# Kernel tuning notes

Hardware: AMD Instinct MI355X
Metric: run time of the kernel (lower is better)

The kernel has to match this reference:

```python
import jax, jax.numpy as jnp
import numpy as np

B, L, D = 2, 2048, 2048
NUM_HEADS, NUM_KV_HEADS, HEAD_DIM = 8, 4, 256
GROUPS = NUM_HEADS // NUM_KV_HEADS
ROPE_BASE, ROPE_SCALE, ROPE_PROP = 10000.0, 1.0, 1.0
WINDOW = 1024
SOFT_CAP = 50.0
K_MASK = -2.3819763e+38
EPS = 1e-6


def rms_norm(x, scale):
    # RMSNorm(head_dim, with_scale=True, scale_plus_one=False), fp32 internals
    xf = x.astype(jnp.float32)
    var = jnp.mean(jnp.square(xf), axis=-1, keepdims=True)
    return (xf * jax.lax.rsqrt(var + EPS) * scale).astype(x.dtype)


def apply_rope(x, positions):
    # x: [B, L, N, H]; Gemma-style half-split rotation over rope_proportion of H
    H = x.shape[-1]
    rope_dim = int(H * ROPE_PROP)
    half = rope_dim // 2
    freq = ROPE_BASE ** (2.0 * jnp.arange(half, dtype=jnp.float32) / rope_dim)
    t = positions.astype(jnp.float32)[:, :, None] / freq[None, None, :]  # [B,L,half]
    t = t / ROPE_SCALE
    sin = jnp.sin(t)[:, :, None, :]  # [B,L,1,half]
    cos = jnp.cos(t)[:, :, None, :]
    x1 = x[..., :half]
    x2 = x[..., half:rope_dim]
    rotated = jnp.concatenate([x1 * cos - x2 * sin, x2 * cos + x1 * sin], axis=-1)
    if rope_dim < H:
        rotated = jnp.concatenate([rotated, x[..., rope_dim:]], axis=-1)
    return rotated.astype(x.dtype)


def setup_inputs() -> dict:
    key = jax.random.key(0)
    ks = jax.random.split(key, 8)
    x = jax.random.normal(ks[0], (B, L, D), dtype=jnp.float32)
    positions = jnp.broadcast_to(jnp.arange(L, dtype=jnp.int32)[None, :], (B, L))
    attn_mask = jnp.broadcast_to(jnp.tril(jnp.ones((L, L), dtype=bool))[None], (B, L, L))
    s = 0.02
    wq = jax.random.normal(ks[1], (D, NUM_HEADS * HEAD_DIM), dtype=jnp.float32) * s
    wk = jax.random.normal(ks[2], (D, NUM_KV_HEADS * HEAD_DIM), dtype=jnp.float32) * s
    wv = jax.random.normal(ks[3], (D, NUM_KV_HEADS * HEAD_DIM), dtype=jnp.float32) * s
    wo = jax.random.normal(ks[4], (NUM_HEADS * HEAD_DIM, D), dtype=jnp.float32) * s
    q_scale = 1.0 + 0.02 * jax.random.normal(ks[5], (HEAD_DIM,), dtype=jnp.float32)
    k_scale = 1.0 + 0.02 * jax.random.normal(ks[6], (HEAD_DIM,), dtype=jnp.float32)
    return {"x": x, "positions": positions, "attn_mask": attn_mask,
            "wq": wq, "wk": wk, "wv": wv, "wo": wo,
            "q_scale": q_scale, "k_scale": k_scale}


def reference(x, positions, attn_mask, wq, wk, wv, wo, q_scale, k_scale):
    q = (x @ wq).reshape(B, L, NUM_HEADS, HEAD_DIM)
    k = (x @ wk).reshape(B, L, NUM_KV_HEADS, HEAD_DIM)
    v = (x @ wv).reshape(B, L, NUM_KV_HEADS, HEAD_DIM)
    q = rms_norm(q, q_scale)
    k = rms_norm(k, k_scale)
    q = apply_rope(q, positions)
    k = apply_rope(k, positions)
    # query_pre_attn_scalar == 1.0 in source (no-op)
    qg = q.reshape(B, L, NUM_KV_HEADS, GROUPS, HEAD_DIM)
    logits = jnp.einsum('blkgh,bskh->blkgs', qg, k).reshape(B, L, NUM_HEADS, L)
    logits = jnp.tanh(logits / SOFT_CAP) * SOFT_CAP
    # sliding-window mask (LOCAL_SLIDING, no cache -> cache_positions = positions)
    cp = positions[:, None, :]
    pp = positions[:, :, None]
    slide = (cp > pp - WINDOW) & (cp < pp + WINDOW)
    mask = attn_mask & slide  # [B, L, S]
    padded = jnp.where(mask[:, :, None, :], logits, K_MASK)
    probs = jax.nn.softmax(padded, axis=-1).astype(k.dtype)
    pg = probs.reshape(B, L, NUM_KV_HEADS, GROUPS, L)
    out = jnp.einsum('blkgs,bskh->blkgh', pg, v).reshape(B, L, NUM_HEADS * HEAD_DIM)
    return out @ wo
```

## Files before the change

### kernel.cpp

```cpp
#include <hip/hip_runtime.h>
#include <stdint.h>

typedef unsigned short u16;
typedef __bf16 bf16x8 __attribute__((ext_vector_type(8)));
typedef float f32x4 __attribute__((ext_vector_type(4)));

#define SEQ 2048
#define NH 8
#define NKVH 4
#define HD 256
#define WIN 1024
#define NBATCH 2

__device__ __forceinline__ u16 f2bf(float f) {
    union { float f; unsigned u; } v; v.f = f;
    unsigned r = v.u + 0x7FFFu + ((v.u >> 16) & 1u);
    return (u16)(r >> 16);
}
__device__ __forceinline__ float bf2f(u16 h) {
    union { unsigned u; float f; } v; v.u = ((unsigned)h) << 16;
    return v.f;
}
__device__ __forceinline__ bf16x8 ld8(const u16* p) {
    return *reinterpret_cast<const bf16x8*>(p);
}
__device__ __forceinline__ void split2(float f, u16& h, u16& l) {
    h = f2bf(f);
    l = f2bf(f - bf2f(h));
}
__device__ __forceinline__ void gld16(const u16* gp, u16* lp) {
    __builtin_amdgcn_global_load_lds(
        (__attribute__((address_space(1))) unsigned int*)gp,
        (__attribute__((address_space(3))) unsigned int*)lp, 16, 0, 0);
}
#define MFMA16(a, b, c) __builtin_amdgcn_mfma_f32_16x16x32_bf16((a), (b), (c), 0, 0, 0)

__global__ void k_prep(const float* __restrict__ x, u16* __restrict__ xh, u16* __restrict__ xl,
                       const float* __restrict__ wq, u16* __restrict__ wqh, u16* __restrict__ wql,
                       const float* __restrict__ wk, u16* __restrict__ wkh, u16* __restrict__ wkl,
                       const float* __restrict__ wv, u16* __restrict__ wvh,
                       const float* __restrict__ wo, u16* __restrict__ woh) {
    __shared__ float tile[64][65];
    int blk = blockIdx.x;
    const int tid = threadIdx.x;
    if (blk < 8192) {
        int i = (blk * 256 + tid) * 4;
        float4 v = *reinterpret_cast<const float4*>(x + i);
        ushort4 oh, ol;
        split2(v.x, oh.x, ol.x); split2(v.y, oh.y, ol.y);
        split2(v.z, oh.z, ol.z); split2(v.w, oh.w, ol.w);
        *reinterpret_cast<ushort4*>(xh + i) = oh;
        *reinterpret_cast<ushort4*>(xl + i) = ol;
        return;
    }
    blk -= 8192;
    const float* src; u16 *dh, *dl; int ncols, c0, k0;
    if (blk < 1024) {
        src = wq; dh = wqh; dl = wql; ncols = 2048;
        c0 = (blk & 31) * 64; k0 = (blk >> 5) * 64;
    } else if (blk < 1536) {
        blk -= 1024;
        src = wk; dh = wkh; dl = wkl; ncols = 1024;
        c0 = (blk & 15) * 64; k0 = (blk >> 4) * 64;
    } else if (blk < 2048) {
        blk -= 1536;
        src = wv; dh = wvh; dl = nullptr; ncols = 1024;
        c0 = (blk & 15) * 64; k0 = (blk >> 4) * 64;
    } else {
        blk -= 2048;
        src = wo; dh = woh; dl = nullptr; ncols = 2048;
        c0 = (blk & 31) * 64; k0 = (blk >> 5) * 64;
    }
    int tx = tid & 63, ty = tid >> 6;
    #pragma unroll
    for (int r = 0; r < 16; ++r) {
        int k = k0 + ty * 16 + r;
        tile[ty * 16 + r][tx] = src[(size_t)k * ncols + c0 + tx];
    }
    __syncthreads();
    #pragma unroll
    for (int r = 0; r < 16; ++r) {
        int c = c0 + ty * 16 + r;
        float f = tile[tx][ty * 16 + r];
        if (dl) {
            u16 h, l; split2(f, h, l);
            dh[(size_t)c * 2048 + k0 + tx] = h;
            dl[(size_t)c * 2048 + k0 + tx] = l;
        } else {
            dh[(size_t)c * 2048 + k0 + tx] = f2bf(f);
        }
    }
}

__global__ __launch_bounds__(256, 4) void k_gemm(
        const u16* __restrict__ A0, const u16* __restrict__ B0,
        const u16* __restrict__ A1, const u16* __restrict__ B1,
        const u16* __restrict__ A2, const u16* __restrict__ B2,
        float* __restrict__ C, int M, int N, int K, int nseg, int vcol0) {
    __shared__ __align__(16) u16 sA[128 * 64];
    __shared__ __align__(16) u16 sB[128 * 64];
    const int tm = blockIdx.x * 128;
    const int tn = blockIdx.y * 128;
    const int tid = threadIdx.x;
    const int lane = tid & 63;
    const int wave = tid >> 6;
    const int wr = (wave >> 1) * 64;
    const int wc = (wave & 1) * 64;
    const int l16 = lane & 15;
    const int g = lane >> 4;
    const int srow = tid >> 3;
    const int schunk = tid & 7;
    const int nseg_eff = (tn >= vcol0) ? 1 : nseg;
    f32x4 acc[4][4] = {};

    for (int seg = 0; seg < nseg_eff; ++seg) {
        const u16* A = seg == 0 ? A0 : (seg == 1 ? A1 : A2);
        const u16* B = seg == 0 ? B0 : (seg == 1 ? B1 : B2);
        for (int k0 = 0; k0 < K; k0 += 64) {
            __syncthreads();
            #pragma unroll
            for (int i = 0; i < 4; ++i) {
                int row = i * 32 + srow;
                int cs = ((schunk ^ (row & 7)) << 3);
                gld16(A + (size_t)(tm + row) * K + k0 + cs, &sA[i * 2048 + tid * 8]);
                gld16(B + (size_t)(tn + row) * K + k0 + cs, &sB[i * 2048 + tid * 8]);
            }
            __syncthreads();
            #pragma unroll
            for (int kk = 0; kk < 2; ++kk) {
                const int j = kk * 4 + g;
                bf16x8 af[4], bfv[4];
                #pragma unroll
                for (int m = 0; m < 4; ++m) {
                    int r = wr + m * 16 + l16;
                    af[m] = ld8(&sA[r * 64 + ((j ^ (r & 7)) << 3)]);
                }
                #pragma unroll
                for (int n = 0; n < 4; ++n) {
                    int r = wc + n * 16 + l16;
                    bfv[n] = ld8(&sB[r * 64 + ((j ^ (r & 7)) << 3)]);
                }
                #pragma unroll
                for (int m = 0; m < 4; ++m)
                    #pragma unroll
                    for (int n = 0; n < 4; ++n)
                        acc[m][n] = MFMA16(af[m], bfv[n], acc[m][n]);
            }
        }
    }
    int rbase = tm + wr + g * 4;
    int cbase = tn + wc + l16;
    #pragma unroll
    for (int m = 0; m < 4; ++m)
        #pragma unroll
        for (int n = 0; n < 4; ++n)
            #pragma unroll
            for (int r = 0; r < 4; ++r)
                C[(size_t)(rbase + m * 16 + r) * N + cbase + n * 16] = acc[m][n][r];
}

__global__ __launch_bounds__(256, 3) void k_gemm1(
        const u16* __restrict__ Ah, const u16* __restrict__ Al,
        const u16* __restrict__ Bh, const u16* __restrict__ Bl,
        float* __restrict__ C, int M, int N, int K, int vcol0) {
    __shared__ __align__(16) u16 sAh[128 * 64];
    __shared__ __align__(16) u16 sAl[128 * 64];
    __shared__ __align__(16) u16 sB[128 * 64];
    const int tm = blockIdx.x * 128;
    const int tn = blockIdx.y * 128;
    const int tid = threadIdx.x;
    const int lane = tid & 63;
    const int wave = tid >> 6;
    const int wr = (wave >> 1) * 64;
    const int wc = (wave & 1) * 64;
    const int l16 = lane & 15;
    const int g = lane >> 4;
    const int srow = tid >> 3;
    const int schunk = tid & 7;
    const bool qk = (tn < vcol0);
    f32x4 acc[4][4] = {};

    for (int k0 = 0; k0 < K; k0 += 64) {
        __syncthreads();
        #pragma unroll
        for (int i = 0; i < 4; ++i) {
            int row = i * 32 + srow;
            int cs = ((schunk ^ (row & 7)) << 3);
            gld16(Ah + (size_t)(tm + row) * K + k0 + cs, &sAh[i * 2048 + tid * 8]);
            if (qk)
                gld16(Al + (size_t)(tm + row) * K + k0 + cs, &sAl[i * 2048 + tid * 8]);
            gld16(Bh + (size_t)(tn + row) * K + k0 + cs, &sB[i * 2048 + tid * 8]);
        }
        __syncthreads();
        #pragma unroll
        for (int kk = 0; kk < 2; ++kk) {
            const int j = kk * 4 + g;
            bf16x8 bfv[4], af[4];
            #pragma unroll
            for (int n = 0; n < 4; ++n) {
                int r = wc + n * 16 + l16;
                bfv[n] = ld8(&sB[r * 64 + ((j ^ (r & 7)) << 3)]);
            }
            #pragma unroll
            for (int m = 0; m < 4; ++m) {
                int r = wr + m * 16 + l16;
                af[m] = ld8(&sAh[r * 64 + ((j ^ (r & 7)) << 3)]);
            }
            #pragma unroll
            for (int m = 0; m < 4; ++m)
                #pragma unroll
                for (int n = 0; n < 4; ++n)
                    acc[m][n] = MFMA16(af[m], bfv[n], acc[m][n]);
            if (qk) {
                bf16x8 afl[4];
                #pragma unroll
                for (int m = 0; m < 4; ++m) {
                    int r = wr + m * 16 + l16;
                    afl[m] = ld8(&sAl[r * 64 + ((j ^ (r & 7)) << 3)]);
                }
                #pragma unroll
                for (int m = 0; m < 4; ++m)
                    #pragma unroll
                    for (int n = 0; n < 4; ++n)
                        acc[m][n] = MFMA16(afl[m], bfv[n], acc[m][n]);
            }
        }
    }

    if (qk) {
        for (int k0 = 0; k0 < K; k0 += 64) {
            __syncthreads();
            #pragma unroll
            for (int i = 0; i < 4; ++i) {
                int row = i * 32 + srow;
                int cs = ((schunk ^ (row & 7)) << 3);
                gld16(Ah + (size_t)(tm + row) * K + k0 + cs, &sAh[i * 2048 + tid * 8]);
                gld16(Bl + (size_t)(tn + row) * K + k0 + cs, &sB[i * 2048 + tid * 8]);
            }
            __syncthreads();
            #pragma unroll
            for (int kk = 0; kk < 2; ++kk) {
                const int j = kk * 4 + g;
                bf16x8 bfv[4], af[4];
                #pragma unroll
                for (int n = 0; n < 4; ++n) {
                    int r = wc + n * 16 + l16;
                    bfv[n] = ld8(&sB[r * 64 + ((j ^ (r & 7)) << 3)]);
                }
                #pragma unroll
                for (int m = 0; m < 4; ++m) {
                    int r = wr + m * 16 + l16;
                    af[m] = ld8(&sAh[r * 64 + ((j ^ (r & 7)) << 3)]);
                }
                #pragma unroll
                for (int m = 0; m < 4; ++m)
                    #pragma unroll
                    for (int n = 0; n < 4; ++n)
                        acc[m][n] = MFMA16(af[m], bfv[n], acc[m][n]);
            }
        }
    }

    int rbase = tm + wr + g * 4;
    int cbase = tn + wc + l16;
    #pragma unroll
    for (int m = 0; m < 4; ++m)
        #pragma unroll
        for (int n = 0; n < 4; ++n)
            #pragma unroll
            for (int r = 0; r < 4; ++r)
                C[(size_t)(rbase + m * 16 + r) * N + cbase + n * 16] = acc[m][n][r];
}

__global__ void k_nrvt(const float* __restrict__ qkv, const int* __restrict__ pos,
                       const float* __restrict__ qscale, const float* __restrict__ kscale,
                       u16* __restrict__ Qh, u16* __restrict__ Ql,
                       u16* __restrict__ Kh, u16* __restrict__ Kl,
                       u16* __restrict__ VT) {
    __shared__ float tile[64][65];
    const int blk = blockIdx.x;
    const int tid = threadIdx.x;
    if (blk >= 12288) {
        int idx = blk - 12288;
        int t0 = (idx & 31) * 64;
        int d0 = ((idx >> 5) & 3) * 64;
        int bh = idx >> 7;
        int b = bh >> 2, h = bh & 3;
        int tx = tid & 63, ty = tid >> 6;
        #pragma unroll
        for (int r = 0; r < 16; ++r) {
            int t = t0 + ty * 16 + r;
            tile[ty * 16 + r][tx] = qkv[(size_t)(b * SEQ + t) * 4096 + 3072 + h * 256 + d0 + tx];
        }
        __syncthreads();
        #pragma unroll
        for (int r = 0; r < 16; ++r) {
            int d = d0 + ty * 16 + r;
            VT[((size_t)bh * 256 + d) * SEQ + t0 + tx] = f2bf(tile[tx][ty * 16 + r]);
        }
        return;
    }
    int wid = blk * 4 + (tid >> 6);
    int lane = tid & 63;
    const int nq = NBATCH * SEQ * NH;
    const int ntot = NBATCH * SEQ * (NH + NKVH);
    if (wid >= ntot) return;
    const float* scale;
    const float* src;
    u16 *dh, *dl;
    int bt, isq;
    if (wid < nq) {
        int h = wid % NH; bt = wid / NH; isq = 1;
        scale = qscale;
        src = qkv + (size_t)bt * 4096 + h * 256;
        int b = bt >> 11, t = bt & 2047;
        size_t off = (((size_t)b * NH + h) * SEQ + t) * 256;
        dh = Qh + off; dl = Ql + off;
    } else {
        int w2 = wid - nq;
        int h = w2 % NKVH; bt = w2 / NKVH; isq = 0;
        scale = kscale;
        src = qkv + (size_t)bt * 4096 + 2048 + h * 256;
        int b = bt >> 11, t = bt & 2047;
        size_t off = (((size_t)b * NKVH + h) * SEQ + t) * 256;
        dh = Kh + off; dl = Kl + off;
    }
    const int t7 = bt & 7;
    float e[4];
    float ssq = 0.f;
    #pragma unroll
    for (int j = 0; j < 4; ++j) { e[j] = src[lane + 64 * j]; ssq += e[j] * e[j]; }
    #pragma unroll
    for (int off = 1; off < 64; off <<= 1) ssq += __shfl_xor(ssq, off);
    float inv = rsqrtf(ssq * (1.0f / 256.0f) + 1e-6f);
    #pragma unroll
    for (int j = 0; j < 4; ++j) e[j] = e[j] * inv * scale[lane + 64 * j];
    float p = (float)pos[bt];
    float fr0 = powf(10000.0f, (2.0f * lane) * (1.0f / 256.0f));
    float fr1 = powf(10000.0f, (2.0f * (lane + 64)) * (1.0f / 256.0f));
    float s0, c0, s1, c1;
    sincosf(p / fr0, &s0, &c0);
    sincosf(p / fr1, &s1, &c1);
    float rv[4];
    rv[0] = e[0] * c0 - e[2] * s0;
    rv[1] = e[1] * c1 - e[3] * s1;
    rv[2] = e[2] * c0 + e[0] * s0;
    rv[3] = e[3] * c1 + e[1] * s1;
    #pragma unroll
    for (int j = 0; j < 4; ++j) {
        int d = lane + 64 * j;
        int dd = isq ? d : ((((d >> 3) ^ t7) << 3) | (d & 7));
        u16 h, l; split2(rv[j], h, l);
        dh[dd] = h; dl[dd] = l;
    }
}

__global__ __launch_bounds__(256, 2) void k_attn(const u16* __restrict__ Qh, const u16* __restrict__ Ql,
                                                 const u16* __restrict__ Kh, const u16* __restrict__ Kl,
                                                 const u16* __restrict__ VT,
                                                 u16* __restrict__ Out) {
    __shared__ __align__(16) u16 sKh[32 * 256];
    __shared__ __align__(16) u16 sKl[32 * 256];
    __shared__ __align__(16) u16 sV[256 * 32];
    __shared__ __align__(16) u16 pls[4][16][40];

    const int id = blockIdx.x;
    const int xcd = id & 7;
    const int j = id >> 3;
    const int b  = xcd >> 2;
    const int hk = xcd & 3;
    const int hq = hk * 2 + (j & 1);
    const int qt = 31 - (j >> 1);
    const int tid = threadIdx.x;
    const int lane = tid & 63;
    const int wave = tid >> 6;
    const int q0b = qt * 64;
    const int q0 = q0b + wave * 16;
    const int l16 = lane & 15;
    const int g = lane >> 4;

    bf16x8 qfh[8], qfl[8];
    {
        size_t qoff = (((size_t)b * NH + hq) * SEQ + q0 + l16) * 256 + g * 8;
        #pragma unroll
        for (int kk = 0; kk < 8; ++kk) {
            qfh[kk] = ld8(Qh + qoff + kk * 32);
            qfl[kk] = ld8(Ql + qoff + kk * 32);
        }
    }

    float ssum[4] = {0.f, 0.f, 0.f, 0.f};
    f32x4 o[16] = {};

    const u16* kgh = Kh + (((size_t)b * NKVH + hk) * SEQ) * 256;
    const u16* kgl = Kl + (((size_t)b * NKVH + hk) * SEQ) * 256;
    const u16* vg  = VT + ((size_t)(b * NKVH + hk) * 256) * SEQ;

    int s_lo = q0b - (WIN - 1); if (s_lo < 0) s_lo = 0; s_lo &= ~31;
    const int s_hi = q0b + 63;
    const int ntiles = (s_hi - s_lo) / 32 + 1;

    for (int t = 0; t < ntiles; ++t) {
        const int s0 = s_lo + t * 32;
        __syncthreads();
        {
            const u16* srch = kgh + (size_t)s0 * 256 + tid * 8;
            const u16* srcl = kgl + (size_t)s0 * 256 + tid * 8;
            #pragma unroll
            for (int i = 0; i < 4; ++i) {
                gld16(srch + i * 2048, &sKh[i * 2048 + tid * 8]);
                gld16(srcl + i * 2048, &sKl[i * 2048 + tid * 8]);
            }
            const u16* srcv = vg + (size_t)(tid >> 2) * SEQ + s0 + (tid & 3) * 8;
            #pragma unroll
            for (int i = 0; i < 4; ++i)
                gld16(srcv + (size_t)i * 64 * SEQ, &sV[i * 2048 + tid * 8]);
        }
        __syncthreads();

        if (s0 <= q0 + 15 && s0 + 31 >= q0 - (WIN - 1)) {
            f32x4 c[2] = {};
            __builtin_amdgcn_s_setprio(1);
            #pragma unroll
            for (int kk = 0; kk < 8; ++kk) {
                #pragma unroll
                for (int cc = 0; cc < 2; ++cc) {
                    int row = cc * 16 + l16;
                    int slot = ((kk * 4 + g) ^ (row & 7)) << 3;
                    bf16x8 kh = ld8(&sKh[row * 256 + slot]);
                    bf16x8 kl = ld8(&sKl[row * 256 + slot]);
                    c[cc] = MFMA16(qfh[kk], kh, c[cc]);
                    c[cc] = MFMA16(qfl[kk], kh, c[cc]);
                    c[cc] = MFMA16(qfh[kk], kl, c[cc]);
                }
            }
            __builtin_amdgcn_s_setprio(0);

            const bool full = (s0 + 31 <= q0) && (s0 >= q0 + 15 - (WIN - 1));
            #pragma unroll
            for (int r = 0; r < 4; ++r) {
                int qp = q0 + g * 4 + r;
                int row = g * 4 + r;
                #pragma unroll
                for (int cc = 0; cc < 2; ++cc) {
                    float ev = __expf(c[cc][r] * 0.04f);
                    float v = 50.f - 100.f * __builtin_amdgcn_rcpf(ev + 1.f);
                    if (!full) {
                        int sp = s0 + cc * 16 + l16;
                        bool valid = (sp <= qp) && (sp > qp - WIN);
                        v = valid ? v : -1e30f;
                    }
                    float p = __expf(v - 20.f);
                    u16 pb = f2bf(p);
                    pls[wave][row][cc * 16 + l16] = pb;
                    ssum[r] += bf2f(pb);
                }
            }
            bf16x8 pa = ld8(&pls[wave][l16][g * 8]);
            __builtin_amdgcn_s_setprio(1);
            #pragma unroll
            for (int jb = 0; jb < 16; ++jb)
                o[jb] = MFMA16(pa, ld8(&sV[(jb * 16 + l16) * 32 + g * 8]), o[jb]);
            __builtin_amdgcn_s_setprio(0);
        }
    }

    #pragma unroll
    for (int off = 1; off < 16; off <<= 1)
        #pragma unroll
        for (int r = 0; r < 4; ++r) ssum[r] += __shfl_xor(ssum[r], off);
    #pragma unroll
    for (int r = 0; r < 4; ++r) {
        float inv = 1.0f / ssum[r];
        int trow = q0 + g * 4 + r;
        size_t base = ((size_t)(b * SEQ + trow) * NH + hq) * 256 + l16;
        #pragma unroll
        for (int jb = 0; jb < 16; ++jb)
            Out[base + jb * 16] = f2bf(o[jb][r] * inv);
    }
}

extern "C" void kernel_launch(void* const* d_in, const int* in_sizes, int n_in,
                              void* d_out, int out_size, void* d_ws, size_t ws_size,
                              hipStream_t stream) {
    (void)in_sizes; (void)n_in; (void)out_size; (void)ws_size;
    const float* x  = (const float*)d_in[0];
    const int* pos  = (const int*)d_in[1];
    const float* wq = (const float*)d_in[3];
    const float* wk = (const float*)d_in[4];
    const float* wv = (const float*)d_in[5];
    const float* wo = (const float*)d_in[6];
    const float* qs = (const float*)d_in[7];
    const float* ks = (const float*)d_in[8];

    const size_t MX = (size_t)4096 * 2048;
    const size_t MW = (size_t)2048 * 2048;

    u16* xh  = (u16*)d_ws;
    u16* xl  = xh + MX;
    u16* wth = xl + MX;
    u16* wtl = wth + MX;
    u16* woth = wtl + MX;
    u16* wotl = woth + MW;
    float* qkv = (float*)(wotl + MW);

    u16* qbh = xh;
    u16* qbl = qbh + MX;
    u16* kbh = qbl + MX;
    u16* kbl = kbh + MX / 2;
    u16* vt  = kbl + MX / 2;
    u16* ao  = (u16*)qkv;

    k_prep<<<11264, 256, 0, stream>>>(x, xh, xl,
                                      wq, wth, wtl,
                                      wk, wth + MW, wtl + MW,
                                      wv, wth + MW + MW / 2,
                                      wo, woth);
    k_gemm1<<<dim3(32, 32), 256, 0, stream>>>(xh, xl, wth, wtl, qkv,
                                              4096, 4096, 2048, 3072);
    k_nrvt<<<13312, 256, 0, stream>>>(qkv, pos, qs, ks, qbh, qbl, kbh, kbl, vt);
    k_attn<<<512, 256, 0, stream>>>(qbh, qbl, kbh, kbl, vt, ao);
    k_gemm<<<dim3(32, 16), 256, 0, stream>>>(ao, woth, ao, woth, ao, wotl, (float*)d_out,
                                             4096, 2048, 2048, 1, 2048);
}
```

Baseline: 360.8 us.

## Fuse split-bf16 QKV GEMM passes into one K loop with smaller K tile

The QKV projection GEMM, which uses a bf16 hi/lo split for extra precision, previously ran a second full K loop to reload A-hi and multiply it by B-lo. Now all four tiles (A hi/lo, B hi/lo) are staged together in one loop with a K step of 32 and a new swizzle. This removes the redundant second pass over A-hi from global memory and its extra synchronisation. In exchange there are twice as many loop iterations and barriers, each with less MFMA work to hide load latency.

```diff
diff --git a/kernel.cpp b/kernel.cpp
--- a/kernel.cpp
+++ b/kernel.cpp
@@ -163,9 +163,10 @@
         const u16* __restrict__ Ah, const u16* __restrict__ Al,
         const u16* __restrict__ Bh, const u16* __restrict__ Bl,
         float* __restrict__ C, int M, int N, int K, int vcol0) {
-    __shared__ __align__(16) u16 sAh[128 * 64];
-    __shared__ __align__(16) u16 sAl[128 * 64];
-    __shared__ __align__(16) u16 sB[128 * 64];
+    __shared__ __align__(16) u16 sAh[128 * 32];
+    __shared__ __align__(16) u16 sAl[128 * 32];
+    __shared__ __align__(16) u16 sBh[128 * 32];
+    __shared__ __align__(16) u16 sBl[128 * 32];
     const int tm = blockIdx.x * 128;
     const int tn = blockIdx.y * 128;
     const int tid = threadIdx.x;
@@ -175,89 +176,63 @@
     const int wc = (wave & 1) * 64;
     const int l16 = lane & 15;
     const int g = lane >> 4;
-    const int srow = tid >> 3;
-    const int schunk = tid & 7;
     const bool qk = (tn < vcol0);
     f32x4 acc[4][4] = {};
 
-    for (int k0 = 0; k0 < K; k0 += 64) {
+    for (int k0 = 0; k0 < K; k0 += 32) {
         __syncthreads();
         #pragma unroll
-        for (int i = 0; i < 4; ++i) {
-            int row = i * 32 + srow;
-            int cs = ((schunk ^ (row & 7)) << 3);
-            gld16(Ah + (size_t)(tm + row) * K + k0 + cs, &sAh[i * 2048 + tid * 8]);
-            if (qk)
-                gld16(Al + (size_t)(tm + row) * K + k0 + cs, &sAl[i * 2048 + tid * 8]);
-            gld16(Bh + (size_t)(tn + row) * K + k0 + cs, &sB[i * 2048 + tid * 8]);
+        for (int i = 0; i < 2; ++i) {
+            int u = i * 256 + tid;
+            int row = u >> 2, chunk = u & 3;
+            int cs = ((chunk ^ ((row >> 1) & 3)) << 3);
+            gld16(Ah + (size_t)(tm + row) * K + k0 + cs, &sAh[u * 8]);
+            gld16(Bh + (size_t)(tn + row) * K + k0 + cs, &sBh[u * 8]);
+            if (qk) {
+                gld16(Al + (size_t)(tm + row) * K + k0 + cs, &sAl[u * 8]);
+                gld16(Bl + (size_t)(tn + row) * K + k0 + cs, &sBl[u * 8]);
+            }
         }
         __syncthreads();
-        #pragma unroll
-        for (int kk = 0; kk < 2; ++kk) {
-            const int j = kk * 4 + g;
-            bf16x8 bfv[4], af[4];
+        bf16x8 afh[4], bfh[4];
+        #pragma unroll
+        for (int m = 0; m < 4; ++m) {
+            int r = wr + m * 16 + l16;
+            afh[m] = ld8(&sAh[r * 32 + ((g ^ ((r >> 1) & 3)) << 3)]);
+        }
+        #pragma unroll
+        for (int n = 0; n < 4; ++n) {
+            int r = wc + n * 16 + l16;
+            bfh[n] = ld8(&sBh[r * 32 + ((g ^ ((r >> 1) & 3)) << 3)]);
+        }
+        #pragma unroll
+        for (int m = 0; m < 4; ++m)
+            #pragma unroll
+            for (int n = 0; n < 4; ++n)
+                acc[m][n] = MFMA16(afh[m], bfh[n], acc[m][n]);
+        if (qk) {
+            bf16x8 afl[4];
+            #pragma unroll
+            for (int m = 0; m < 4; ++m) {
+                int r = wr + m * 16 + l16;
+                afl[m] = ld8(&sAl[r * 32 + ((g ^ ((r >> 1) & 3)) << 3)]);
+            }
+            #pragma unroll
+            for (int m = 0; m < 4; ++m)
+                #pragma unroll
+                for (int n = 0; n < 4; ++n)
+                    acc[m][n] = MFMA16(afl[m], bfh[n], acc[m][n]);
+            bf16x8 bfl[4];
             #pragma unroll
             for (int n = 0; n < 4; ++n) {
                 int r = wc + n * 16 + l16;
-                bfv[n] = ld8(&sB[r * 64 + ((j ^ (r & 7)) << 3)]);
-            }
-            #pragma unroll
-            for (int m = 0; m < 4; ++m) {
-                int r = wr + m * 16 + l16;
-                af[m] = ld8(&sAh[r * 64 + ((j ^ (r & 7)) << 3)]);
+                bfl[n] = ld8(&sBl[r * 32 + ((g ^ ((r >> 1) & 3)) << 3)]);
             }
             #pragma unroll
             for (int m = 0; m < 4; ++m)
                 #pragma unroll
                 for (int n = 0; n < 4; ++n)
-                    acc[m][n] = MFMA16(af[m], bfv[n], acc[m][n]);
-            if (qk) {
-                bf16x8 afl[4];
-                #pragma unroll
-                for (int m = 0; m < 4; ++m) {
-                    int r = wr + m * 16 + l16;
-                    afl[m] = ld8(&sAl[r * 64 + ((j ^ (r & 7)) << 3)]);
-                }
-                #pragma unroll
-                for (int m = 0; m < 4; ++m)
-                    #pragma unroll
-                    for (int n = 0; n < 4; ++n)
-                        acc[m][n] = MFMA16(afl[m], bfv[n], acc[m][n]);
-            }
-        }
-    }
-
-    if (qk) {
-        for (int k0 = 0; k0 < K; k0 += 64) {
-            __syncthreads();
-            #pragma unroll
-            for (int i = 0; i < 4; ++i) {
-                int row = i * 32 + srow;
-                int cs = ((schunk ^ (row & 7)) << 3);
-                gld16(Ah + (size_t)(tm + row) * K + k0 + cs, &sAh[i * 2048 + tid * 8]);
-                gld16(Bl + (size_t)(tn + row) * K + k0 + cs, &sB[i * 2048 + tid * 8]);
-            }
-            __syncthreads();
-            #pragma unroll
-            for (int kk = 0; kk < 2; ++kk) {
-                const int j = kk * 4 + g;
-                bf16x8 bfv[4], af[4];
-                #pragma unroll
-                for (int n = 0; n < 4; ++n) {
-                    int r = wc + n * 16 + l16;
-                    bfv[n] = ld8(&sB[r * 64 + ((j ^ (r & 7)) << 3)]);
-                }
-                #pragma unroll
-                for (int m = 0; m < 4; ++m) {
-                    int r = wr + m * 16 + l16;
-                    af[m] = ld8(&sAh[r * 64 + ((j ^ (r & 7)) << 3)]);
-                }
-                #pragma unroll
-                for (int m = 0; m < 4; ++m)
-                    #pragma unroll
-                    for (int n = 0; n < 4; ++n)
-                        acc[m][n] = MFMA16(af[m], bfv[n], acc[m][n]);
-            }
+                    acc[m][n] = MFMA16(afh[m], bfl[n], acc[m][n]);
         }
     }
 
```

After: 370.8 us. +2.8%, slower.
